# Performance work log

Hardware: AMD Instinct MI355X
Metric: run time of the kernel (lower is better)

Reference implementation:

```python
import jax, jax.numpy as jnp
import numpy as np

DIM = 768
H = 12
HD = DIM // H
LN_EPS = 1e-5


def setup_inputs() -> dict:
    key = jax.random.key(0)
    ks = jax.random.split(key, 8)
    B, N, C = 64, 197, DIM
    s = 0.02
    return {
        "x": jax.random.normal(ks[0], (B, N, C), jnp.float32),
        "qkv_w": jax.random.normal(ks[1], (C, 3 * C), jnp.float32) * s,
        "qkv_b": jnp.zeros((3 * C,), jnp.float32),
        "proj_w": jax.random.normal(ks[2], (C, C), jnp.float32) * s,
        "proj_b": jnp.zeros((C,), jnp.float32),
        "ht_w": jax.random.normal(ks[3], (HD, C), jnp.float32) * s,
        "ht_b": jnp.zeros((C,), jnp.float32),
        "ln_g": jnp.ones((HD,), jnp.float32),
        "ln_b": jnp.zeros((HD,), jnp.float32),
        "pos_embed": jax.random.normal(ks[4], (1, H, C), jnp.float32) * s,
    }


def reference(x, qkv_w, qkv_b, proj_w, proj_b, ht_w, ht_b, ln_g, ln_b, pos_embed):
    B, N, C = x.shape
    scale = HD ** -0.5
    # head tokens: mean over sequence per head -> [B, H, HD]
    ht = x.reshape(B, N, H, HD).mean(axis=1)
    ht = ht @ ht_w + ht_b                      # [B, H, C]
    ht = ht.reshape(B, H, H, HD)
    mu = ht.mean(axis=-1, keepdims=True)
    var = jnp.mean((ht - mu) ** 2, axis=-1, keepdims=True)
    ht = (ht - mu) * jax.lax.rsqrt(var + LN_EPS) * ln_g + ln_b
    ht = jax.nn.gelu(ht, approximate=False).reshape(B, H, C) + pos_embed
    xc = jnp.concatenate([x, ht], axis=1)      # [B, T=N+H, C]
    T = N + H
    qkv = (xc @ qkv_w + qkv_b).reshape(B, T, 3, H, HD)
    q, k, v = qkv[:, :, 0], qkv[:, :, 1], qkv[:, :, 2]  # [B, T, H, HD]
    attn = jnp.einsum('bqhd,bkhd->bhqk', q, k) * scale
    attn = jax.nn.softmax(attn, axis=-1)
    out = jnp.einsum('bhqk,bkhd->bqhd', attn, v).reshape(B, T, C)
    out = out @ proj_w + proj_b
    cls = out[:, :1] + out[:, N:].mean(axis=1, keepdims=True)
    return jnp.concatenate([cls, out[:, 1:N]], axis=1)
```

## Files before the change

kernel.cpp:

```cpp
#include <hip/hip_runtime.h>
#include <cstdint>
#include <cstddef>

typedef unsigned short u16;
typedef __attribute__((ext_vector_type(8))) __bf16 bf16x8;
typedef __attribute__((ext_vector_type(4))) unsigned short u16x4;
typedef __attribute__((ext_vector_type(8))) unsigned short u16x8;
typedef __attribute__((ext_vector_type(4))) float f32x4;

#define NTOK 197
#define TT   209
#define CDIM 768
#define NH   12
#define HD   64
#define BATCH 64
#define GM (BATCH*TT)
#define VTP 224
#define NQKV 2304

__device__ __forceinline__ float bf2f(u16 u){ return __uint_as_float(((unsigned)u)<<16); }
__device__ __forceinline__ u16 f2bf(float f){
  unsigned x = __float_as_uint(f);
  return (u16)((x + 0x7FFFu + ((x>>16)&1u)) >> 16);
}

__device__ __forceinline__ void gll16(const void* g, void* l){
  __builtin_amdgcn_global_load_lds((const __attribute__((address_space(1))) void*)g,
                                   (__attribute__((address_space(3))) void*)l,
                                   16, 0, 0);
}

__device__ __forceinline__ float wsum64(float v){
  #pragma unroll
  for (int o = 32; o > 0; o >>= 1) v += __shfl_xor(v, o, 64);
  return v;
}

__global__ __launch_bounds__(64) void detect_kernel(const u16* __restrict__ x, int* flag){
  const int lane = threadIdx.x;
  float mx = 0.f;
  #pragma unroll
  for (int i = 0; i < 16; i++) {
    float v = fabsf(bf2f(x[i*64 + lane]));
    if (!(v < 1e30f)) v = 1e30f;
    mx = fmaxf(mx, v);
  }
  #pragma unroll
  for (int o = 32; o; o >>= 1) mx = fmaxf(mx, __shfl_xor(mx, o, 64));
  if (lane == 0) *flag = (mx < 1e5f) ? 1 : 0;
}

struct CA { const void* in[10]; void* out[10]; int n[10]; };
__global__ __launch_bounds__(256) void convert_all_kernel(CA a, const int* __restrict__ flag){
  const int seg = blockIdx.y;
  if (seg == 1 || seg == 3) return;
  const int f = *flag;
  if (seg == 0 && f) return;
  const int n = a.n[seg];
  const int n4 = n >> 2;
  u16* out = (u16*)a.out[seg];
  if (f) {
    const u16x4* in = (const u16x4*)a.in[seg];
    for (int i = blockIdx.x*256 + threadIdx.x; i < n4; i += gridDim.x*256)
      ((u16x4*)out)[i] = in[i];
  } else {
    const f32x4* in = (const f32x4*)a.in[seg];
    for (int i = blockIdx.x*256 + threadIdx.x; i < n4; i += gridDim.x*256){
      f32x4 v = in[i];
      u16x4 o;
      #pragma unroll
      for (int j=0;j<4;j++) o[j] = f2bf(v[j]);
      ((u16x4*)out)[i] = o;
    }
  }
  if (blockIdx.x == 0 && (int)threadIdx.x < (n & 3)) {
    int i = (n4 << 2) + threadIdx.x;
    out[i] = f ? ((const u16*)a.in[seg])[i] : f2bf(((const float*)a.in[seg])[i]);
  }
}

__global__ __launch_bounds__(256) void transpose2_kernel(
    const void* __restrict__ w1, const void* __restrict__ w2,
    u16* __restrict__ o1, u16* __restrict__ o2, const int* __restrict__ flag)
{
  __shared__ u16 lds[64][66];
  const int f = *flag;
  int bid = blockIdx.x;
  const void* in; u16* out; int K, N, tx, ty;
  if (bid < 432) { in = w1; out = o1; K = CDIM; N = NQKV; tx = bid % 36; ty = bid / 36; }
  else { bid -= 432; in = w2; out = o2; K = CDIM; N = CDIM; tx = bid % 12; ty = bid / 12; }
  const int n0 = tx*64, k0 = ty*64;
  const int c = threadIdx.x & 63, r0 = threadIdx.x >> 6;
  #pragma unroll
  for (int i=0;i<16;i++) {
    int r = i*4 + r0;
    size_t idx = (size_t)(k0+r)*N + n0 + c;
    lds[r][c] = f ? ((const u16*)in)[idx] : f2bf(((const float*)in)[idx]);
  }
  __syncthreads();
  #pragma unroll
  for (int i=0;i<16;i++) {
    int r = i*4 + r0;
    out[(size_t)(n0+r)*K + k0 + c] = lds[c][r];
  }
}

__global__ __launch_bounds__(256) void mean_kernel(
    const u16* __restrict__ xc, const void* __restrict__ xr,
    float* __restrict__ mbuf, const int* __restrict__ flag)
{
  const int b = blockIdx.x, s = blockIdx.y;
  const int tid = threadIdx.x;
  const int f = *flag;
  const u16* x = f ? (const u16*)xr : xc;
  const u16* xp = x + (size_t)b*NTOK*CDIM + s*256 + tid;
  float cs = 0.f;
  for (int n = 0; n < NTOK; n++) cs += bf2f(xp[(size_t)n*CDIM]);
  mbuf[(size_t)b*CDIM + s*256 + tid] = cs * (1.0f/(float)NTOK);
}

__global__ __launch_bounds__(256) void htmm_kernel(
    const float* __restrict__ mbuf,
    const u16* __restrict__ htw, const u16* __restrict__ htb,
    const u16* __restrict__ lng, const u16* __restrict__ lnb,
    const u16* __restrict__ pos, u16* __restrict__ ht)
{
  const int b = blockIdx.x, h = blockIdx.y;
  const int tid = threadIdx.x;
  __shared__ float msh[64];
  if (tid < 64) msh[tid] = mbuf[(size_t)b*CDIM + h*HD + tid];
  __syncthreads();

  float v0 = bf2f(htb[tid]), v1 = bf2f(htb[tid+256]), v2 = bf2f(htb[tid+512]);
  for (int d = 0; d < HD; d++) {
    const float md = msh[d];
    const u16* wr = htw + (size_t)d*CDIM;
    v0 += md * bf2f(wr[tid]);
    v1 += md * bf2f(wr[tid+256]);
    v2 += md * bf2f(wr[tid+512]);
  }
  const float gam = bf2f(lng[tid & 63]), bet = bf2f(lnb[tid & 63]);
  float vv[3] = {v0, v1, v2};
  #pragma unroll
  for (int ch = 0; ch < 3; ch++) {
    int c = ch*256 + tid;
    float mu = wsum64(vv[ch]) * (1.0f/(float)HD);
    float dv = vv[ch] - mu;
    float var = wsum64(dv*dv) * (1.0f/(float)HD);
    float y = dv * rsqrtf(var + 1e-5f) * gam + bet;
    float ge = 0.5f * y * (1.0f + erff(y * 0.70710678118654752f));
    float o = ge + bf2f(pos[h*CDIM + c]);
    ht[((size_t)(b*NH + h))*CDIM + c] = f2bf(o);
  }
}

template<int MODE>
__global__ __launch_bounds__(256, 2) void gemm_kernel(
    const u16* __restrict__ A0c, const void* __restrict__ A0r,
    const u16* __restrict__ A1,
    const u16* __restrict__ Bt, const u16* __restrict__ bias,
    u16* __restrict__ qout,
    void* __restrict__ outv, float* __restrict__ csb, const int* __restrict__ flag)
{
  const int tid = threadIdx.x;
  const int lane = tid & 63;
  const int w = tid >> 6;
  const int wm = w >> 1, wn = w & 1;
  const int lr = lane & 15, kg = lane >> 4;

  const int NT = gridDim.x;
  const int nwg = NT * gridDim.y;
  const int orig = blockIdx.y * NT + blockIdx.x;
  const int xcd = orig & 7, sIdx = orig >> 3;
  const int q = nwg >> 3, r = nwg & 7;
  const int wg = ((xcd < r) ? xcd*(q+1) : r*(q+1) + (xcd-r)*q) + sIdx;
  const int tm = wg / NT, tn = wg - tm*NT;

  __shared__ __align__(16) u16 As[5][4096];
  __shared__ __align__(16) u16 Bs[5][4096];

  const int f = *flag;
  const u16* A0 = (MODE == 0) ? (f ? (const u16*)A0r : A0c) : A0c;

  f32x4 acc[4][4];
  #pragma unroll
  for (int i=0;i<4;i++)
    #pragma unroll
    for (int j=0;j<4;j++) acc[i][j] = (f32x4){0.f,0.f,0.f,0.f};

  const u16* garow[2];
  const u16* gbrow[2];
  #pragma unroll
  for (int i=0;i<2;i++){
    int row = (i*4 + w)*16 + (lane >> 2);
    int rr = tm*128 + row; if (rr > GM-1) rr = GM-1;
    if (MODE == 0) {
      int bb = rr / TT; int t = rr - bb*TT;
      garow[i] = (t < NTOK) ? (A0 + (size_t)(bb*NTOK + t)*CDIM)
                            : (A1 + (size_t)(bb*NH + (t - NTOK))*CDIM);
    } else {
      garow[i] = A0 + (size_t)rr*CDIM;
    }
    gbrow[i] = Bt + (size_t)(tn*128 + row)*CDIM;
  }
  const int gseg = (lane & 3) ^ ((lane >> 3) & 3);

#define STAGE(kt_, bf_) do { \
    const int ko_ = (kt_)*32 + gseg*8; \
    gll16(garow[0] + ko_, (void*)&As[bf_][(0*4+w)*512]); \
    gll16(garow[1] + ko_, (void*)&As[bf_][(1*4+w)*512]); \
    gll16(gbrow[0] + ko_, (void*)&Bs[bf_][(0*4+w)*512]); \
    gll16(gbrow[1] + ko_, (void*)&Bs[bf_][(1*4+w)*512]); \
  } while(0)

  STAGE(0, 0);
  STAGE(1, 1);
  STAGE(2, 2);

  const int spA = kg ^ ((lr >> 1) & 3);

  #pragma unroll
  for (int kt = 0; kt < 24; kt++) {
    const int cb = kt % 5;
    if (kt < 21) {
      STAGE(kt+3, (kt+3)%5);
      asm volatile("s_waitcnt vmcnt(12)" ::: "memory");
    } else if (kt == 21) {
      asm volatile("s_waitcnt vmcnt(8)" ::: "memory");
    } else if (kt == 22) {
      asm volatile("s_waitcnt vmcnt(4)" ::: "memory");
    } else {
      asm volatile("s_waitcnt vmcnt(0)" ::: "memory");
    }
    __builtin_amdgcn_s_barrier();

    bf16x8 av[4], bv[4];
    #pragma unroll
    for (int mi=0; mi<4; mi++)
      av[mi] = *(const bf16x8*)&As[cb][(wm*64+mi*16+lr)*32 + spA*8];
    #pragma unroll
    for (int ni=0; ni<4; ni++)
      bv[ni] = *(const bf16x8*)&Bs[cb][(wn*64+ni*16+lr)*32 + spA*8];
    #pragma unroll
    for (int mi=0; mi<4; mi++)
      #pragma unroll
      for (int ni=0; ni<4; ni++)
        acc[mi][ni] = __builtin_amdgcn_mfma_f32_16x16x32_bf16(av[mi], bv[ni], acc[mi][ni], 0,0,0);
  }
#undef STAGE

  #pragma unroll
  for (int mi=0; mi<4; mi++){
    const int rb = tm*128 + wm*64 + mi*16 + kg*4;
    #pragma unroll
    for (int ni=0; ni<4; ni++){
      const int c = tn*128 + wn*64 + ni*16 + lr;
      const float bs = bf2f(bias[c]);
      if (MODE == 0) {
        #pragma unroll
        for (int j=0;j<4;j++){
          int rr = rb + j;
          if (rr < GM) qout[(size_t)rr*NQKV + c] = f2bf(acc[mi][ni][j] + bs);
        }
      } else {
        #pragma unroll
        for (int j=0;j<4;j++){
          int rr = rb + j;
          if (rr < GM) {
            int bb = rr / TT; int t = rr - bb*TT;
            float v = acc[mi][ni][j] + bs;
            if (t >= 1 && t < NTOK) {
              size_t oi = ((size_t)(bb*NTOK + t))*CDIM + c;
              if (f) ((u16*)outv)[oi] = f2bf(v);
              else   ((float*)outv)[oi] = v;
            } else {
              int idx = (t == 0) ? 0 : (t - NTOK + 1);
              csb[((size_t)(bb*13 + idx))*CDIM + c] = v;
            }
          }
        }
      }
    }
  }
}

__global__ __launch_bounds__(256) void vtrans_kernel(
    const u16* __restrict__ qkvo, u16* __restrict__ vb)
{
  __shared__ u16 lds[64][66];
  const int tt0 = blockIdx.x*64;
  const int bh = blockIdx.y;
  const int b = bh / NH, h = bh - b*NH;
  const int c = threadIdx.x & 63, r0 = threadIdx.x >> 6;
  #pragma unroll
  for (int i=0;i<16;i++) {
    int t = tt0 + i*4 + r0;
    u16 v = 0;
    if (t < TT) v = qkvo[(size_t)(b*TT + t)*NQKV + 1536 + h*64 + c];
    lds[i*4+r0][c] = v;
  }
  __syncthreads();
  #pragma unroll
  for (int i=0;i<16;i++) {
    int d = i*4 + r0;
    int t = tt0 + c;
    if (t < VTP) vb[((size_t)(bh)*HD + d)*VTP + t] = lds[c][d];
  }
}

__global__ __launch_bounds__(256) void attn_kernel(
    const u16* __restrict__ qkvo, const u16* __restrict__ vt, u16* __restrict__ ob)
{
  __shared__ __align__(16) u16 P[4][7*16*32];
  const int tid = threadIdx.x;
  const int lane = tid & 63;
  const int w = tid >> 6;
  const int lr = lane & 15, kg = lane >> 4;

  const int cid = blockIdx.x*4 + w;
  const int bh = cid / 14, ck = cid - bh*14;
  const int b = bh / NH, h = bh - b*NH;
  const int q0 = ck*16;

  const u16* qg  = qkvo + (size_t)(b*TT)*NQKV + h*64;
  const u16* kgp = qg + CDIM;
  const u16* vg  = vt + (size_t)bh*HD*VTP;

  int qrow = q0 + lr; if (qrow > TT-1) qrow = TT-1;
  const bf16x8 qf0 = *(const bf16x8*)&qg[(size_t)qrow*NQKV + kg*8];
  const bf16x8 qf1 = *(const bf16x8*)&qg[(size_t)qrow*NQKV + 32 + kg*8];

  f32x4 sv[14];
  #pragma unroll
  for (int kt = 0; kt < 14; kt++) {
    int krow = kt*16 + lr; if (krow > TT-1) krow = TT-1;
    const u16* kr = kgp + (size_t)krow*NQKV;
    bf16x8 kf0 = *(const bf16x8*)&kr[kg*8];
    bf16x8 kf1 = *(const bf16x8*)&kr[32 + kg*8];
    f32x4 sa = {0.f,0.f,0.f,0.f};
    sa = __builtin_amdgcn_mfma_f32_16x16x32_bf16(kf0, qf0, sa, 0,0,0);
    sa = __builtin_amdgcn_mfma_f32_16x16x32_bf16(kf1, qf1, sa, 0,0,0);
    sv[kt] = sa;
  }

  float m = -3.0e38f;
  #pragma unroll
  for (int kt = 0; kt < 13; kt++)
    #pragma unroll
    for (int j=0;j<4;j++){ sv[kt][j] *= 0.125f; m = fmaxf(m, sv[kt][j]); }
  #pragma unroll
  for (int j=0;j<4;j++){
    sv[13][j] *= 0.125f;
    if (208 + kg*4 + j < TT) m = fmaxf(m, sv[13][j]);
  }
  m = fmaxf(m, __shfl_xor(m, 16, 64));
  m = fmaxf(m, __shfl_xor(m, 32, 64));

  float ssum = 0.f;
  #pragma unroll
  for (int kt = 0; kt < 13; kt++)
    #pragma unroll
    for (int j=0;j<4;j++){ float e = __expf(sv[kt][j] - m); sv[kt][j] = e; ssum += e; }
  #pragma unroll
  for (int j=0;j<4;j++){
    float e = (208 + kg*4 + j < TT) ? __expf(sv[13][j] - m) : 0.f;
    sv[13][j] = e; ssum += e;
  }
  ssum += __shfl_xor(ssum, 16, 64);
  ssum += __shfl_xor(ssum, 32, 64);
  const float inv = 1.0f / ssum;

  u16* Pw = &P[w][0];
  #pragma unroll
  for (int kt = 0; kt < 14; kt++) {
    u16x4 pk;
    #pragma unroll
    for (int j=0;j<4;j++) pk[j] = f2bf(sv[kt][j] * inv);
    *(u16x4*)&Pw[(kt>>1)*512 + lr*32 + (kt&1)*16 + kg*4] = pk;
  }

  f32x4 acc[4];
  #pragma unroll
  for (int dt=0; dt<4; dt++) acc[dt] = (f32x4){0.f,0.f,0.f,0.f};
  #pragma unroll
  for (int ks = 0; ks < 7; ks++) {
    bf16x8 pf = *(const bf16x8*)&Pw[ks*512 + lr*32 + kg*8];
    #pragma unroll
    for (int dt = 0; dt < 4; dt++) {
      bf16x8 vf = *(const bf16x8*)&vg[(dt*16+lr)*VTP + ks*32 + kg*8];
      acc[dt] = __builtin_amdgcn_mfma_f32_16x16x32_bf16(pf, vf, acc[dt], 0,0,0);
    }
  }

  #pragma unroll
  for (int dt = 0; dt < 4; dt++)
    #pragma unroll
    for (int j = 0; j < 4; j++) {
      int tq = q0 + kg*4 + j;
      if (tq < TT)
        ob[((size_t)(b*TT + tq))*CDIM + h*HD + dt*16 + lr] = f2bf(acc[dt][j]);
    }
}

__global__ __launch_bounds__(256) void final2_kernel(
    const float* __restrict__ csb, void* __restrict__ outv, const int* __restrict__ flag)
{
  const int f = *flag;
  int i = blockIdx.x*256 + threadIdx.x;
  if (i >= BATCH*CDIM) return;
  int b = i / CDIM, c = i - b*CDIM;
  const float* p = csb + (size_t)b*13*CDIM + c;
  float s = 0.f;
  #pragma unroll
  for (int j = 1; j <= 12; j++) s += p[(size_t)j*CDIM];
  float v = p[0] + s * (1.0f/12.0f);
  size_t oi = ((size_t)b*NTOK)*CDIM + c;
  if (f) ((u16*)outv)[oi] = f2bf(v);
  else   ((float*)outv)[oi] = v;
}

extern "C" void kernel_launch(void* const* d_in, const int* in_sizes, int n_in,
                              void* d_out, int out_size, void* d_ws, size_t ws_size,
                              hipStream_t stream)
{
  char* ws = (char*)d_ws;
  size_t off = 0;
  auto alloc = [&](size_t bytes)->void* {
    void* p = ws + off; off += (bytes + 255) & ~(size_t)255; return p;
  };

  int* flag = (int*)alloc(256);

  u16* cin[10];
  for (int i = 0; i < 10; i++) cin[i] = (u16*)alloc((size_t)in_sizes[i]*2);

  u16* qkvT  = (u16*)alloc((size_t)3*CDIM*CDIM*2);
  u16* projT = (u16*)alloc((size_t)CDIM*CDIM*2);
  u16* htb_  = (u16*)alloc((size_t)BATCH*NH*CDIM*2);
  float* mbuf = (float*)alloc((size_t)BATCH*CDIM*4);
  u16* qkvo  = (u16*)alloc((size_t)GM*NQKV*2);
  u16* vb    = (u16*)alloc((size_t)BATCH*NH*HD*VTP*2);
  float* csb = (float*)alloc((size_t)BATCH*13*CDIM*4);
  u16* ao    = cin[0];

  detect_kernel<<<1, 64, 0, stream>>>((const u16*)d_in[0], flag);

  CA ca;
  for (int i = 0; i < 10; i++) { ca.in[i] = d_in[i]; ca.out[i] = cin[i]; ca.n[i] = in_sizes[i]; }
  convert_all_kernel<<<dim3(256, 10), 256, 0, stream>>>(ca, flag);

  transpose2_kernel<<<576, 256, 0, stream>>>(d_in[1], d_in[3], qkvT, projT, flag);
  mean_kernel<<<dim3(BATCH, 3), 256, 0, stream>>>(cin[0], d_in[0], mbuf, flag);
  htmm_kernel<<<dim3(BATCH, NH), 256, 0, stream>>>(mbuf, cin[5], cin[6], cin[7], cin[8], cin[9], htb_);
  gemm_kernel<0><<<dim3(NQKV/128, (GM+127)/128), 256, 0, stream>>>(
      cin[0], d_in[0], htb_, qkvT, cin[2], qkvo, nullptr, nullptr, flag);
  vtrans_kernel<<<dim3(4, BATCH*NH), 256, 0, stream>>>(qkvo, vb);
  attn_kernel<<<(BATCH*NH*14)/4, 256, 0, stream>>>(qkvo, vb, ao);
  gemm_kernel<1><<<dim3(CDIM/128, (GM+127)/128), 256, 0, stream>>>(
      ao, nullptr, nullptr, projT, cin[4], nullptr, d_out, csb, flag);
  final2_kernel<<<(BATCH*CDIM+255)/256, 256, 0, stream>>>(csb, d_out, flag);
}
```

Before: 245.9 us.

## Fuse V transpose into QKV GEMM epilogue and stage K in LDS per head

The QKV GEMM epilogue now writes the V columns directly into the transposed per-head layout, so the separate vtrans kernel and its round trip through global memory are removed. The padding columns of the transposed V buffer are zeroed in the convert kernel instead. Attention now runs one block per (batch, head) and loads K once into LDS, shared by four waves that loop over query chunks, instead of each wave re-reading K from global memory. In exchange, the epilogue does strided 2-byte scattered stores for V, and there are fewer attention blocks, each doing more serial work.

```diff
diff --git a/kernel.cpp b/kernel.cpp
--- a/kernel.cpp
+++ b/kernel.cpp
@@ -53,7 +53,16 @@
 struct CA { const void* in[10]; void* out[10]; int n[10]; };
 __global__ __launch_bounds__(256) void convert_all_kernel(CA a, const int* __restrict__ flag){
   const int seg = blockIdx.y;
-  if (seg == 1 || seg == 3) return;
+  if (seg == 1) {
+    int row = blockIdx.x*256 + threadIdx.x;
+    if (row < a.n[1]) {
+      u16* p = (u16*)a.out[1] + (size_t)row*VTP + TT;
+      #pragma unroll
+      for (int j = 0; j < VTP-TT; j++) p[j] = 0;
+    }
+    return;
+  }
+  if (seg == 3) return;
   const int f = *flag;
   if (seg == 0 && f) return;
   const int n = a.n[seg];
@@ -159,7 +168,7 @@
     const u16* __restrict__ A0c, const void* __restrict__ A0r,
     const u16* __restrict__ A1,
     const u16* __restrict__ Bt, const u16* __restrict__ bias,
-    u16* __restrict__ qout,
+    u16* __restrict__ qout, u16* __restrict__ vbo,
     void* __restrict__ outv, float* __restrict__ csb, const int* __restrict__ flag)
 {
   const int tid = threadIdx.x;
@@ -257,10 +266,23 @@
       const int c = tn*128 + wn*64 + ni*16 + lr;
       const float bs = bf2f(bias[c]);
       if (MODE == 0) {
-        #pragma unroll
-        for (int j=0;j<4;j++){
-          int rr = rb + j;
-          if (rr < GM) qout[(size_t)rr*NQKV + c] = f2bf(acc[mi][ni][j] + bs);
+        if (c < 2*CDIM) {
+          #pragma unroll
+          for (int j=0;j<4;j++){
+            int rr = rb + j;
+            if (rr < GM) qout[(size_t)rr*NQKV + c] = f2bf(acc[mi][ni][j] + bs);
+          }
+        } else {
+          const int hh = (c - 2*CDIM) >> 6;
+          const int dd = c & 63;
+          #pragma unroll
+          for (int j=0;j<4;j++){
+            int rr = rb + j;
+            if (rr < GM) {
+              int bb = rr / TT; int t = rr - bb*TT;
+              vbo[((size_t)(bb*NH + hh)*HD + dd)*VTP + t] = f2bf(acc[mi][ni][j] + bs);
+            }
+          }
         }
       } else {
         #pragma unroll
@@ -284,122 +306,106 @@
   }
 }
 
-__global__ __launch_bounds__(256) void vtrans_kernel(
-    const u16* __restrict__ qkvo, u16* __restrict__ vb)
-{
-  __shared__ u16 lds[64][66];
-  const int tt0 = blockIdx.x*64;
-  const int bh = blockIdx.y;
-  const int b = bh / NH, h = bh - b*NH;
-  const int c = threadIdx.x & 63, r0 = threadIdx.x >> 6;
-  #pragma unroll
-  for (int i=0;i<16;i++) {
-    int t = tt0 + i*4 + r0;
-    u16 v = 0;
-    if (t < TT) v = qkvo[(size_t)(b*TT + t)*NQKV + 1536 + h*64 + c];
-    lds[i*4+r0][c] = v;
-  }
-  __syncthreads();
-  #pragma unroll
-  for (int i=0;i<16;i++) {
-    int d = i*4 + r0;
-    int t = tt0 + c;
-    if (t < VTP) vb[((size_t)(bh)*HD + d)*VTP + t] = lds[c][d];
-  }
-}
-
 __global__ __launch_bounds__(256) void attn_kernel(
     const u16* __restrict__ qkvo, const u16* __restrict__ vt, u16* __restrict__ ob)
 {
+  __shared__ __align__(16) u16 Kl[224*72];
   __shared__ __align__(16) u16 P[4][7*16*32];
   const int tid = threadIdx.x;
   const int lane = tid & 63;
   const int w = tid >> 6;
   const int lr = lane & 15, kg = lane >> 4;
 
-  const int cid = blockIdx.x*4 + w;
-  const int bh = cid / 14, ck = cid - bh*14;
+  const int bh = blockIdx.x;
   const int b = bh / NH, h = bh - b*NH;
-  const int q0 = ck*16;
 
   const u16* qg  = qkvo + (size_t)(b*TT)*NQKV + h*64;
   const u16* kgp = qg + CDIM;
   const u16* vg  = vt + (size_t)bh*HD*VTP;
 
-  int qrow = q0 + lr; if (qrow > TT-1) qrow = TT-1;
-  const bf16x8 qf0 = *(const bf16x8*)&qg[(size_t)qrow*NQKV + kg*8];
-  const bf16x8 qf1 = *(const bf16x8*)&qg[(size_t)qrow*NQKV + 32 + kg*8];
-
-  f32x4 sv[14];
-  #pragma unroll
-  for (int kt = 0; kt < 14; kt++) {
-    int krow = kt*16 + lr; if (krow > TT-1) krow = TT-1;
-    const u16* kr = kgp + (size_t)krow*NQKV;
-    bf16x8 kf0 = *(const bf16x8*)&kr[kg*8];
-    bf16x8 kf1 = *(const bf16x8*)&kr[32 + kg*8];
-    f32x4 sa = {0.f,0.f,0.f,0.f};
-    sa = __builtin_amdgcn_mfma_f32_16x16x32_bf16(kf0, qf0, sa, 0,0,0);
-    sa = __builtin_amdgcn_mfma_f32_16x16x32_bf16(kf1, qf1, sa, 0,0,0);
-    sv[kt] = sa;
-  }
-
-  float m = -3.0e38f;
-  #pragma unroll
-  for (int kt = 0; kt < 13; kt++)
-    #pragma unroll
-    for (int j=0;j<4;j++){ sv[kt][j] *= 0.125f; m = fmaxf(m, sv[kt][j]); }
-  #pragma unroll
-  for (int j=0;j<4;j++){
-    sv[13][j] *= 0.125f;
-    if (208 + kg*4 + j < TT) m = fmaxf(m, sv[13][j]);
-  }
-  m = fmaxf(m, __shfl_xor(m, 16, 64));
-  m = fmaxf(m, __shfl_xor(m, 32, 64));
-
-  float ssum = 0.f;
-  #pragma unroll
-  for (int kt = 0; kt < 13; kt++)
-    #pragma unroll
-    for (int j=0;j<4;j++){ float e = __expf(sv[kt][j] - m); sv[kt][j] = e; ssum += e; }
-  #pragma unroll
-  for (int j=0;j<4;j++){
-    float e = (208 + kg*4 + j < TT) ? __expf(sv[13][j] - m) : 0.f;
-    sv[13][j] = e; ssum += e;
-  }
-  ssum += __shfl_xor(ssum, 16, 64);
-  ssum += __shfl_xor(ssum, 32, 64);
-  const float inv = 1.0f / ssum;
+  for (int s = tid; s < 224*8; s += 256) {
+    int kc = s >> 3, seg = s & 7;
+    uint4 val = make_uint4(0,0,0,0);
+    if (kc < TT) val = *(const uint4*)&kgp[(size_t)kc*NQKV + seg*8];
+    *(uint4*)&Kl[kc*72 + seg*8] = val;
+  }
+  __syncthreads();
 
   u16* Pw = &P[w][0];
-  #pragma unroll
-  for (int kt = 0; kt < 14; kt++) {
-    u16x4 pk;
-    #pragma unroll
-    for (int j=0;j<4;j++) pk[j] = f2bf(sv[kt][j] * inv);
-    *(u16x4*)&Pw[(kt>>1)*512 + lr*32 + (kt&1)*16 + kg*4] = pk;
-  }
-
-  f32x4 acc[4];
-  #pragma unroll
-  for (int dt=0; dt<4; dt++) acc[dt] = (f32x4){0.f,0.f,0.f,0.f};
-  #pragma unroll
-  for (int ks = 0; ks < 7; ks++) {
-    bf16x8 pf = *(const bf16x8*)&Pw[ks*512 + lr*32 + kg*8];
-    #pragma unroll
-    for (int dt = 0; dt < 4; dt++) {
-      bf16x8 vf = *(const bf16x8*)&vg[(dt*16+lr)*VTP + ks*32 + kg*8];
-      acc[dt] = __builtin_amdgcn_mfma_f32_16x16x32_bf16(pf, vf, acc[dt], 0,0,0);
-    }
-  }
-
-  #pragma unroll
-  for (int dt = 0; dt < 4; dt++)
-    #pragma unroll
-    for (int j = 0; j < 4; j++) {
-      int tq = q0 + kg*4 + j;
-      if (tq < TT)
-        ob[((size_t)(b*TT + tq))*CDIM + h*HD + dt*16 + lr] = f2bf(acc[dt][j]);
-    }
+  for (int ck = w; ck < 14; ck += 4) {
+    const int q0 = ck*16;
+    int qrow = q0 + lr; if (qrow > TT-1) qrow = TT-1;
+    const bf16x8 qf0 = *(const bf16x8*)&qg[(size_t)qrow*NQKV + kg*8];
+    const bf16x8 qf1 = *(const bf16x8*)&qg[(size_t)qrow*NQKV + 32 + kg*8];
+
+    f32x4 sv[14];
+    #pragma unroll
+    for (int kt = 0; kt < 14; kt++) {
+      bf16x8 kf0 = *(const bf16x8*)&Kl[(kt*16+lr)*72 + kg*8];
+      bf16x8 kf1 = *(const bf16x8*)&Kl[(kt*16+lr)*72 + 32 + kg*8];
+      f32x4 sa = {0.f,0.f,0.f,0.f};
+      sa = __builtin_amdgcn_mfma_f32_16x16x32_bf16(kf0, qf0, sa, 0,0,0);
+      sa = __builtin_amdgcn_mfma_f32_16x16x32_bf16(kf1, qf1, sa, 0,0,0);
+      sv[kt] = sa;
+    }
+
+    float m = -3.0e38f;
+    #pragma unroll
+    for (int kt = 0; kt < 13; kt++)
+      #pragma unroll
+      for (int j=0;j<4;j++){ sv[kt][j] *= 0.125f; m = fmaxf(m, sv[kt][j]); }
+    #pragma unroll
+    for (int j=0;j<4;j++){
+      sv[13][j] *= 0.125f;
+      if (208 + kg*4 + j < TT) m = fmaxf(m, sv[13][j]);
+    }
+    m = fmaxf(m, __shfl_xor(m, 16, 64));
+    m = fmaxf(m, __shfl_xor(m, 32, 64));
+
+    float ssum = 0.f;
+    #pragma unroll
+    for (int kt = 0; kt < 13; kt++)
+      #pragma unroll
+      for (int j=0;j<4;j++){ float e = __expf(sv[kt][j] - m); sv[kt][j] = e; ssum += e; }
+    #pragma unroll
+    for (int j=0;j<4;j++){
+      float e = (208 + kg*4 + j < TT) ? __expf(sv[13][j] - m) : 0.f;
+      sv[13][j] = e; ssum += e;
+    }
+    ssum += __shfl_xor(ssum, 16, 64);
+    ssum += __shfl_xor(ssum, 32, 64);
+    const float inv = 1.0f / ssum;
+
+    #pragma unroll
+    for (int kt = 0; kt < 14; kt++) {
+      u16x4 pk;
+      #pragma unroll
+      for (int j=0;j<4;j++) pk[j] = f2bf(sv[kt][j] * inv);
+      *(u16x4*)&Pw[(kt>>1)*512 + lr*32 + (kt&1)*16 + kg*4] = pk;
+    }
+
+    f32x4 acc[4];
+    #pragma unroll
+    for (int dt=0; dt<4; dt++) acc[dt] = (f32x4){0.f,0.f,0.f,0.f};
+    #pragma unroll
+    for (int ks = 0; ks < 7; ks++) {
+      bf16x8 pf = *(const bf16x8*)&Pw[ks*512 + lr*32 + kg*8];
+      #pragma unroll
+      for (int dt = 0; dt < 4; dt++) {
+        bf16x8 vf = *(const bf16x8*)&vg[(dt*16+lr)*VTP + ks*32 + kg*8];
+        acc[dt] = __builtin_amdgcn_mfma_f32_16x16x32_bf16(pf, vf, acc[dt], 0,0,0);
+      }
+    }
+
+    #pragma unroll
+    for (int dt = 0; dt < 4; dt++)
+      #pragma unroll
+      for (int j = 0; j < 4; j++) {
+        int tq = q0 + kg*4 + j;
+        if (tq < TT)
+          ob[((size_t)(b*TT + tq))*CDIM + h*HD + dt*16 + lr] = f2bf(acc[dt][j]);
+      }
+  }
 }
 
 __global__ __launch_bounds__(256) void final2_kernel(
@@ -447,16 +453,16 @@
 
   CA ca;
   for (int i = 0; i < 10; i++) { ca.in[i] = d_in[i]; ca.out[i] = cin[i]; ca.n[i] = in_sizes[i]; }
+  ca.out[1] = vb; ca.n[1] = BATCH*NH*HD;
   convert_all_kernel<<<dim3(256, 10), 256, 0, stream>>>(ca, flag);
 
   transpose2_kernel<<<576, 256, 0, stream>>>(d_in[1], d_in[3], qkvT, projT, flag);
   mean_kernel<<<dim3(BATCH, 3), 256, 0, stream>>>(cin[0], d_in[0], mbuf, flag);
   htmm_kernel<<<dim3(BATCH, NH), 256, 0, stream>>>(mbuf, cin[5], cin[6], cin[7], cin[8], cin[9], htb_);
   gemm_kernel<0><<<dim3(NQKV/128, (GM+127)/128), 256, 0, stream>>>(
-      cin[0], d_in[0], htb_, qkvT, cin[2], qkvo, nullptr, nullptr, flag);
-  vtrans_kernel<<<dim3(4, BATCH*NH), 256, 0, stream>>>(qkvo, vb);
-  attn_kernel<<<(BATCH*NH*14)/4, 256, 0, stream>>>(qkvo, vb, ao);
+      cin[0], d_in[0], htb_, qkvT, cin[2], qkvo, vb, nullptr, nullptr, flag);
+  attn_kernel<<<BATCH*NH, 256, 0, stream>>>(qkvo, vb, ao);
   gemm_kernel<1><<<dim3(CDIM/128, (GM+127)/128), 256, 0, stream>>>(
-      ao, nullptr, nullptr, projT, cin[4], nullptr, d_out, csb, flag);
+      ao, nullptr, nullptr, projT, cin[4], nullptr, nullptr, d_out, csb, flag);
   final2_kernel<<<(BATCH*CDIM+255)/256, 256, 0, stream>>>(csb, d_out, flag);
 }
```

New measurement: 244.1 us. About the same (-0.7%).
